# Kernel tuning notes

Measured on AMD Instinct MI355X. Metric: run time of the kernel, lower is better.

## Reference

```python
import jax, jax.numpy as jnp
import numpy as np

B, IMG, P, C, DEPTH, NCLS = 8, 224, 16, 96, 12, 43
H = W = IMG // P
L = H * W            # 196 tokens
D = 2 * C            # d_inner, ssm_ratio=2
N = 16               # d_state
R = (C + 15) // 16   # dt_rank = ceil(96/16) = 6
K = 4                # scan directions


def _ln(x, w, b, eps=1e-6):
    mu = x.mean(-1, keepdims=True)
    var = ((x - mu) ** 2).mean(-1, keepdims=True)
    return (x - mu) * jax.lax.rsqrt(var + eps) * w + b


def setup_inputs() -> dict:
    key = jax.random.key(0)
    ks = jax.random.split(key, 16)
    def nrm(k, shape, s=0.02):
        return jax.random.normal(k, shape, jnp.float32) * s
    return {
        "x": jax.random.normal(ks[0], (B, 3, IMG, IMG), jnp.float32),
        "patch_w": nrm(ks[1], (C, 3, P, P)),
        "patch_b": jnp.zeros((C,), jnp.float32),
        "pos_embed": nrm(ks[2], (1, L, C)),
        "ln1_w": jnp.ones((DEPTH, C), jnp.float32),
        "ln1_b": jnp.zeros((DEPTH, C), jnp.float32),
        "in_proj_w": nrm(ks[3], (DEPTH, C, 2 * D)),
        "conv_w": nrm(ks[4], (DEPTH, D, 1, 3, 3), 0.1),
        "conv_b": jnp.zeros((DEPTH, D), jnp.float32),
        "x_proj_w": nrm(ks[5], (DEPTH, K, R + 2 * N, D)),
        "dt_proj_w": nrm(ks[6], (DEPTH, K, D, R), R ** -0.5),
        "dt_proj_b": jnp.full((DEPTH, K, D), float(np.log(np.expm1(0.01))), jnp.float32),
        "A_logs": jnp.tile(jnp.log(jnp.arange(1, N + 1, dtype=jnp.float32)), (DEPTH, K, D, 1)),
        "Ds": jnp.ones((DEPTH, K, D), jnp.float32),
        "out_norm_w": jnp.ones((DEPTH, D), jnp.float32),
        "out_norm_b": jnp.zeros((DEPTH, D), jnp.float32),
        "out_proj_w": nrm(ks[7], (DEPTH, D, C)),
        "norm_w": jnp.ones((C,), jnp.float32),
        "norm_b": jnp.zeros((C,), jnp.float32),
        "head_w": nrm(ks[8], (C, NCLS)),
        "head_b": jnp.zeros((NCLS,), jnp.float32),
    }


def _ss2d(x, in_w, cw, cb, xpw, dtw, dtb, Alog, Dsk, onw, onb, ow):
    # x: (B,H,W,C)  -- SS2D 'v2' forward
    xz = x @ in_w                          # (B,H,W,2D)
    xa, z = jnp.split(xz, 2, axis=-1)
    xc = jnp.transpose(xa, (0, 3, 1, 2))   # (B,D,H,W)
    xc = jax.lax.conv_general_dilated(xc, cw, (1, 1), "SAME",
        dimension_numbers=("NCHW", "OIHW", "NCHW"), feature_group_count=D)
    xc = jax.nn.silu(xc + cb[None, :, None, None])
    # cross-scan: 4 traversal orders (row-major, col-major, and their reverses)
    x1 = xc.reshape(-1, D, L)
    x2 = jnp.transpose(xc, (0, 1, 3, 2)).reshape(-1, D, L)
    xs = jnp.stack([x1, x2, x1[..., ::-1], x2[..., ::-1]], 1)   # (B,K,D,L)
    dbl = jnp.einsum("bkdl,kcd->bkcl", xs, xpw)
    dts, Bs, Cs = jnp.split(dbl, [R, R + N], axis=2)            # (B,K,R,L),(B,K,N,L),(B,K,N,L)
    dts = jnp.einsum("bkrl,kdr->bkdl", dts, dtw)
    dts = jax.nn.softplus(dts + dtb[None, :, :, None])
    A = -jnp.exp(Alog)                                          # (K,D,N)
    # selective scan over token axis (sequential recurrence)
    seq = (jnp.moveaxis(xs, -1, 0), jnp.moveaxis(dts, -1, 0),
           jnp.moveaxis(Bs, -1, 0), jnp.moveaxis(Cs, -1, 0))
    h0 = jnp.zeros(xs.shape[:3] + (N,), xs.dtype)               # (B,K,D,N)
    def step(h, t):
        x_t, dt_t, B_t, C_t = t
        h = h * jnp.exp(dt_t[..., None] * A) + (dt_t * x_t)[..., None] * B_t[:, :, None, :]
        return h, jnp.einsum("bkdn,bkn->bkd", h, C_t)
    _, ys = jax.lax.scan(step, h0, seq)
    ys = jnp.moveaxis(ys, 0, -1)                                # (B,K,D,L)
    ys = ys + Dsk[None, :, :, None] * xs
    # cross-merge: undo reverses/transpose and sum the 4 directions
    y = ys[:, 0] + ys[:, 2, :, ::-1]
    yt = ys[:, 1] + ys[:, 3, :, ::-1]
    y = y + jnp.transpose(yt.reshape(-1, D, W, H), (0, 1, 3, 2)).reshape(-1, D, L)
    y = jnp.transpose(y.reshape(-1, D, H, W), (0, 2, 3, 1))     # (B,H,W,D)
    y = _ln(y, onw, onb)
    y = y * jax.nn.silu(z)
    return y @ ow


def reference(x, patch_w, patch_b, pos_embed, ln1_w, ln1_b, in_proj_w, conv_w, conv_b,
              x_proj_w, dt_proj_w, dt_proj_b, A_logs, Ds, out_norm_w, out_norm_b,
              out_proj_w, norm_w, norm_b, head_w, head_b):
    # patch embed: 16x16 stride-16 conv -> (B, L, C)
    t = jax.lax.conv_general_dilated(x, patch_w, (P, P), "VALID",
        dimension_numbers=("NCHW", "OIHW", "NCHW")) + patch_b[None, :, None, None]
    t = jnp.transpose(t.reshape(-1, C, L), (0, 2, 1)) + pos_embed
    t = t.reshape(-1, H, W, C)
    for i in range(DEPTH):
        t = t + _ss2d(_ln(t, ln1_w[i], ln1_b[i]), in_proj_w[i], conv_w[i], conv_b[i],
                      x_proj_w[i], dt_proj_w[i], dt_proj_b[i], A_logs[i], Ds[i],
                      out_norm_w[i], out_norm_b[i], out_proj_w[i])
    t = _ln(t.reshape(-1, L, C), norm_w, norm_b)
    return t.mean(1) @ head_w + head_b
```

## Files before the change

kernel.cpp:

```cpp
#include <hip/hip_runtime.h>
#include <math.h>

#define BB 8
#define IMGS 224
#define PSZ 16
#define CC 96
#define DEPTH 12
#define NCLS 43
#define HH 14
#define WW 14
#define LL 196
#define DD 192
#define NSTATE 16
#define RRANK 6
#define KDIR 4
#define DBLC 38
#define NSEG 16
#define PTOK 4
#define TSTR 200
#define OFF_B 1200
#define OFF_C 4336
#define DBKSZ 7552
#define XT 14
#define XPAD 196
#define GT 4
#define YSTRIDE (BB * DD * LL)

__device__ __forceinline__ float wave_sum(float v) {
#pragma unroll
  for (int m = 32; m; m >>= 1) v += __shfl_xor(v, m, 64);
  return v;
}

__device__ __forceinline__ float silu_f(float x) {
  return x / (1.f + __expf(-x));
}

__global__ void k_patch(const float* __restrict__ x, const float* __restrict__ pw,
                        const float* __restrict__ pb, const float* __restrict__ pos,
                        float* __restrict__ t) {
  __shared__ float s_x[PTOK][768];
  int tok0 = blockIdx.x * PTOK;
  for (int tk = 0; tk < PTOK; tk++) {
    int tok = tok0 + tk;
    int b = tok / LL, l = tok % LL;
    int ph = l / WW, pwc = l % WW;
    for (int e = threadIdx.x; e < 768; e += 128) {
      int ci = e >> 8, kh = (e >> 4) & 15, kw = e & 15;
      s_x[tk][e] = x[((size_t)(b * 3 + ci) * IMGS + ph * PSZ + kh) * IMGS + pwc * PSZ + kw];
    }
  }
  __syncthreads();
  if (threadIdx.x < CC) {
    int c = threadIdx.x;
    float a0 = pb[c], a1 = a0, a2 = a0, a3 = a0;
    const float* wr = pw + (size_t)c * 768;
    for (int e = 0; e < 768; e++) {
      float wv = wr[e];
      a0 += s_x[0][e] * wv;
      a1 += s_x[1][e] * wv;
      a2 += s_x[2][e] * wv;
      a3 += s_x[3][e] * wv;
    }
    float acc[4] = {a0, a1, a2, a3};
    for (int tk = 0; tk < PTOK; tk++) {
      int tok = tok0 + tk;
      t[(size_t)tok * CC + c] = acc[tk] + pos[(tok % LL) * CC + c];
    }
  }
}

__global__ void k_lnproj(const float* __restrict__ t, const float* __restrict__ w,
                         const float* __restrict__ bias, const float* __restrict__ ipw,
                         float* __restrict__ xa, float* __restrict__ z) {
  __shared__ float s_x[CC];
  int tok = blockIdx.x;
  int tid = threadIdx.x;
  if (tid < 64) {
    int lane = tid;
    const float* p = t + (size_t)tok * CC;
    float v0 = p[lane];
    float v1 = (lane < CC - 64) ? p[lane + 64] : 0.f;
    float mu = wave_sum(v0 + v1) * (1.f / CC);
    float d0 = v0 - mu;
    float d1 = (lane < CC - 64) ? (v1 - mu) : 0.f;
    float var = wave_sum(d0 * d0 + d1 * d1) * (1.f / CC);
    float rs = rsqrtf(var + 1e-6f);
    s_x[lane] = d0 * rs * w[lane] + bias[lane];
    if (lane < CC - 64) s_x[lane + 64] = d1 * rs * w[lane + 64] + bias[lane + 64];
  }
  __syncthreads();
  int j = tid;
  float acc = 0.f;
  for (int c = 0; c < CC; c++) acc += s_x[c] * ipw[(size_t)c * (2 * DD) + j];
  if (j < DD) xa[(size_t)tok * DD + j] = acc;
  else z[(size_t)tok * DD + (j - DD)] = acc;
}

__global__ __launch_bounds__(256, 4) void k_xproj(
    const float* __restrict__ xa, const float* __restrict__ cw,
    const float* __restrict__ cb, const float* __restrict__ xpw,
    float* __restrict__ xcT, float* __restrict__ dbl) {
  __shared__ float s_w[DBLC * DD];
  __shared__ float s_x[XT * XPAD];
  int lt = blockIdx.x;
  int k = blockIdx.y;
  int b = blockIdx.z;
  int tid = threadIdx.x;
  int l0 = lt * XT;

  const float4* wsrc = (const float4*)(xpw + (size_t)k * DBLC * DD);
  float4* wdst = (float4*)s_w;
  for (int idx = tid; idx < (DBLC * DD) / 4; idx += 256) wdst[idx] = wsrc[idx];

  for (int idx = tid; idx < XT * (DD / 4); idx += 256) {
    int i = idx / (DD / 4);
    int d = (idx % (DD / 4)) * 4;
    int l = l0 + i;
    int lr = (k >= 2) ? (LL - 1 - l) : l;
    int src = (k & 1) ? ((lr % HH) * WW + lr / HH) : lr;
    int h = src / WW, w = src % WW;
    const float4 bv = *(const float4*)(cb + d);
    float a0 = bv.x, a1 = bv.y, a2 = bv.z, a3 = bv.w;
    if (h >= 1 && h < HH - 1 && w >= 1 && w < WW - 1) {
#pragma unroll
      for (int kh = 0; kh < 3; kh++) {
#pragma unroll
        for (int kw = 0; kw < 3; kw++) {
          const float4 v = *(const float4*)(
              xa + ((size_t)(b * LL + (h + kh - 1) * WW + (w + kw - 1))) * DD + d);
          int wo = kh * 3 + kw;
          a0 += v.x * cw[(d + 0) * 9 + wo];
          a1 += v.y * cw[(d + 1) * 9 + wo];
          a2 += v.z * cw[(d + 2) * 9 + wo];
          a3 += v.w * cw[(d + 3) * 9 + wo];
        }
      }
    } else {
      for (int kh = 0; kh < 3; kh++) {
        int hh = h + kh - 1;
        if (hh < 0 || hh >= HH) continue;
        for (int kw = 0; kw < 3; kw++) {
          int ww = w + kw - 1;
          if (ww < 0 || ww >= WW) continue;
          const float4 v = *(const float4*)(xa + ((size_t)(b * LL + hh * WW + ww)) * DD + d);
          int wo = kh * 3 + kw;
          a0 += v.x * cw[(d + 0) * 9 + wo];
          a1 += v.y * cw[(d + 1) * 9 + wo];
          a2 += v.z * cw[(d + 2) * 9 + wo];
          a3 += v.w * cw[(d + 3) * 9 + wo];
        }
      }
    }
    float4 r = make_float4(silu_f(a0), silu_f(a1), silu_f(a2), silu_f(a3));
    *(float4*)(s_x + i * XPAD + d) = r;
    if (k == 0) *(float4*)(xcT + ((size_t)(b * LL) + src) * DD + d) = r;
  }
  __syncthreads();

  int li = tid & 15;
  int cbi = tid >> 4;
  if (li >= XT) return;
  int l = l0 + li;
  float* base = dbl + (size_t)(b * KDIR + k) * DBKSZ;
  const float4* xr = (const float4*)(s_x + li * XPAD);
  const float4* w0 = (const float4*)(s_w + cbi * DD);
  const float4* w1 = (const float4*)(s_w + (cbi + 16) * DD);
  bool has2 = (cbi < DBLC - 32);
  const float4* w2 = has2 ? (const float4*)(s_w + (cbi + 32) * DD) : w0;
  float a0 = 0.f, a1 = 0.f, a2 = 0.f;
#pragma unroll 8
  for (int q = 0; q < DD / 4; q++) {
    float4 a = xr[q];
    float4 v0 = w0[q], v1 = w1[q], v2 = w2[q];
    a0 += a.x * v0.x + a.y * v0.y + a.z * v0.z + a.w * v0.w;
    a1 += a.x * v1.x + a.y * v1.y + a.z * v1.z + a.w * v1.w;
    a2 += a.x * v2.x + a.y * v2.y + a.z * v2.z + a.w * v2.w;
  }
  {
    int c = cbi;
    if (c < RRANK) base[c * TSTR + l] = a0;
    else base[OFF_B + l * NSTATE + (c - RRANK)] = a0;
  }
  {
    int c = cbi + 16;
    if (c < RRANK + NSTATE) base[OFF_B + l * NSTATE + (c - RRANK)] = a1;
    else base[OFF_C + (c - RRANK - NSTATE) * TSTR + l] = a1;
  }
  if (has2) {
    int c = cbi + 32;
    base[OFF_C + (c - RRANK - NSTATE) * TSTR + l] = a2;
  }
}

__global__ __launch_bounds__(256, 4) void k_scan(
    const float* __restrict__ xcT, const float* __restrict__ dbl,
    const float* __restrict__ dtw, const float* __restrict__ dtb,
    const float* __restrict__ alog, const float* __restrict__ dsv,
    float* __restrict__ ysum) {
  __shared__ float s_h[2][NSTATE][LL + 1];
  __shared__ float s_dt[2][LL];
  __shared__ float s_u[2][LL];
  __shared__ float s_xv[2][LL];
  __shared__ float s_cumdt[2][LL];
  __shared__ unsigned short s_src[LL];
  __shared__ float s_hin[2][NSEG][NSTATE];
  __shared__ float s_hend[2][NSEG][NSTATE];
  __shared__ float s_cum[2][NSEG][NSTATE];
  __shared__ float s_segsum[2][NSEG];
  __shared__ float s_A[2][NSTATE];
  __shared__ float s_y[2][LL];
  int tid = threadIdx.x;
  int s = tid >> 4;
  int n = tid & 15;
  int bd = blockIdx.x;
  int dp = bd % (DD / 2);
  int d0 = dp * 2;
  int b = bd / (DD / 2);
  int k = blockIdx.y;

  int len = (s < 4) ? 13 : 12;
  int l0 = s * 12 + ((s < 4) ? s : 4);

  float A0 = -__expf(alog[((size_t)k * DD + d0) * NSTATE + n]);
  float A1 = -__expf(alog[((size_t)k * DD + d0 + 1) * NSTATE + n]);
  float Dsc0 = dsv[k * DD + d0];
  float Dsc1 = dsv[k * DD + d0 + 1];
  const float* blp = dbl + (size_t)(b * KDIR + k) * DBKSZ;
  if (tid < NSTATE) { s_A[0][tid] = A0; s_A[1][tid] = A1; }

  if (tid < LL) {
    int l = tid;
    float r[RRANK];
#pragma unroll
    for (int rr = 0; rr < RRANK; rr++) r[rr] = blp[rr * TSTR + l];
    const float* wp0 = dtw + ((size_t)k * DD + d0) * RRANK;
    const float* wp1 = wp0 + RRANK;
    float m0 = dtb[k * DD + d0], m1 = dtb[k * DD + d0 + 1];
#pragma unroll
    for (int rr = 0; rr < RRANK; rr++) { m0 += r[rr] * wp0[rr]; m1 += r[rr] * wp1[rr]; }
    float dt0 = (m0 > 20.f) ? m0 : __logf(1.f + __expf(m0));
    float dt1 = (m1 > 20.f) ? m1 : __logf(1.f + __expf(m1));
    int lr = (k >= 2) ? (LL - 1 - l) : l;
    int src = (k & 1) ? ((lr % HH) * WW + lr / HH) : lr;
    float2 xv = *(const float2*)(xcT + ((size_t)b * LL + src) * DD + d0);
    s_dt[0][l] = dt0; s_dt[1][l] = dt1;
    s_u[0][l] = dt0 * xv.x; s_u[1][l] = dt1 * xv.y;
    s_xv[0][l] = xv.x; s_xv[1][l] = xv.y;
    s_src[l] = (unsigned short)src;
  }
  __syncthreads();

  if (tid < LL) {
    int l = tid;
    int myseg = (l < 52) ? (l / 13) : (4 + (l - 52) / 12);
    int sl0 = myseg * 12 + ((myseg < 4) ? myseg : 4);
    float a0 = 0.f, a1 = 0.f;
    for (int j = sl0; j <= l; j++) { a0 += s_dt[0][j]; a1 += s_dt[1][j]; }
    s_cumdt[0][l] = a0; s_cumdt[1][l] = a1;
    int slen = (myseg < 4) ? 13 : 12;
    if (l == sl0 + slen - 1) { s_segsum[0][myseg] = a0; s_segsum[1][myseg] = a1; }
  }
  __syncthreads();

  float Breg[13];
#pragma unroll
  for (int i = 0; i < 13; i++) {
    int li = (i < len) ? (l0 + i) : l0;
    Breg[i] = blp[OFF_B + li * NSTATE + n];
  }
  float h0 = 0.f, h1 = 0.f;
#pragma unroll
  for (int i = 0; i < 13; i++) {
    if (i < len) {
      int l = l0 + i;
      float a0 = __expf(s_dt[0][l] * A0);
      float a1 = __expf(s_dt[1][l] * A1);
      h0 = h0 * a0 + s_u[0][l] * Breg[i];
      h1 = h1 * a1 + s_u[1][l] * Breg[i];
      s_h[0][n][l] = h0;
      s_h[1][n][l] = h1;
    }
  }
  s_hend[0][s][n] = h0; s_hend[1][s][n] = h1;
  s_cum[0][s][n] = __expf(A0 * s_segsum[0][s]);
  s_cum[1][s][n] = __expf(A1 * s_segsum[1][s]);
  __syncthreads();

  {
    float hh0 = 0.f, hh1 = 0.f;
    for (int ss = 0; ss < s; ss++) {
      hh0 = s_cum[0][ss][n] * hh0 + s_hend[0][ss][n];
      hh1 = s_cum[1][ss][n] * hh1 + s_hend[1][ss][n];
    }
    s_hin[0][s][n] = hh0; s_hin[1][s][n] = hh1;
  }
  __syncthreads();

  if (tid < LL) {
    int l = tid;
    int myseg = (l < 52) ? (l / 13) : (4 + (l - 52) / 12);
    float cd0 = s_cumdt[0][l], cd1 = s_cumdt[1][l];
    const float* q = blp + OFF_C + l;
    float y0 = 0.f, y1 = 0.f;
#pragma unroll
    for (int nn = 0; nn < NSTATE; nn++) {
      float Cv = q[nn * TSTR];
      float hf0 = s_h[0][nn][l] + __expf(s_A[0][nn] * cd0) * s_hin[0][myseg][nn];
      float hf1 = s_h[1][nn][l] + __expf(s_A[1][nn] * cd1) * s_hin[1][myseg][nn];
      y0 += hf0 * Cv;
      y1 += hf1 * Cv;
    }
    y0 += Dsc0 * s_xv[0][l];
    y1 += Dsc1 * s_xv[1][l];
    int src = s_src[l];
    s_y[0][src] = y0;
    s_y[1][src] = y1;
  }
  __syncthreads();
  if (tid < LL) {
    size_t base = (size_t)k * YSTRIDE + ((size_t)b * DD + d0) * LL;
    ysum[base + tid] = s_y[0][tid];
    ysum[base + LL + tid] = s_y[1][tid];
  }
}

__global__ void k_gateproj(const float* __restrict__ ys,
                           const float* __restrict__ onw, const float* __restrict__ onb,
                           const float* __restrict__ z, const float* __restrict__ opw,
                           float* __restrict__ t,
                           const float* __restrict__ nlw, const float* __restrict__ nlb,
                           const float* __restrict__ ipw,
                           float* __restrict__ xa, float* __restrict__ zout, int mode) {
  __shared__ float s_g[GT][DD];
  __shared__ float s_t[GT][CC];
  __shared__ float s_x[GT][CC];
  __shared__ float s_p[4][GT][CC];
  int tok0 = blockIdx.x * GT;
  int b = tok0 / LL;
  int l0 = tok0 % LL;
  int tid = threadIdx.x;

  if (tid < DD) {
    size_t base = ((size_t)b * DD + tid) * LL + l0;
    float4 v0 = *(const float4*)(ys + base);
    float4 v1 = *(const float4*)(ys + (size_t)YSTRIDE + base);
    float4 v2 = *(const float4*)(ys + 2 * (size_t)YSTRIDE + base);
    float4 v3 = *(const float4*)(ys + 3 * (size_t)YSTRIDE + base);
    s_g[0][tid] = v0.x + v1.x + v2.x + v3.x;
    s_g[1][tid] = v0.y + v1.y + v2.y + v3.y;
    s_g[2][tid] = v0.z + v1.z + v2.z + v3.z;
    s_g[3][tid] = v0.w + v1.w + v2.w + v3.w;
  }
  __syncthreads();

  {
    int w = tid >> 6;
    int lane = tid & 63;
    if (w < GT) {
      int tok = tok0 + w;
      float v0 = s_g[w][lane];
      float v1 = s_g[w][lane + 64];
      float v2 = s_g[w][lane + 128];
      float mu = wave_sum(v0 + v1 + v2) * (1.f / DD);
      float d0 = v0 - mu, d1 = v1 - mu, d2 = v2 - mu;
      float var = wave_sum(d0 * d0 + d1 * d1 + d2 * d2) * (1.f / DD);
      float rs = rsqrtf(var + 1e-6f);
      const float* zp = z + (size_t)tok * DD;
      s_g[w][lane]       = (d0 * rs * onw[lane] + onb[lane]) * silu_f(zp[lane]);
      s_g[w][lane + 64]  = (d1 * rs * onw[lane + 64] + onb[lane + 64]) * silu_f(zp[lane + 64]);
      s_g[w][lane + 128] = (d2 * rs * onw[lane + 128] + onb[lane + 128]) * silu_f(zp[lane + 128]);
    }
  }
  __syncthreads();

  {
    int c = tid % CC;
    int part = tid / CC;
    int dlo = part * 48;
    float a0 = 0.f, a1 = 0.f, a2 = 0.f, a3 = 0.f;
#pragma unroll 8
    for (int j = 0; j < 48; j++) {
      float wv = opw[(size_t)(dlo + j) * CC + c];
      a0 += s_g[0][dlo + j] * wv;
      a1 += s_g[1][dlo + j] * wv;
      a2 += s_g[2][dlo + j] * wv;
      a3 += s_g[3][dlo + j] * wv;
    }
    s_p[part][0][c] = a0;
    s_p[part][1][c] = a1;
    s_p[part][2][c] = a2;
    s_p[part][3][c] = a3;
  }
  __syncthreads();
  {
    int tk = tid / CC;
    int c = tid % CC;
    float tn = t[(size_t)(tok0 + tk) * CC + c] +
               s_p[0][tk][c] + s_p[1][tk][c] + s_p[2][tk][c] + s_p[3][tk][c];
    t[(size_t)(tok0 + tk) * CC + c] = tn;
    s_t[tk][c] = tn;
  }
  __syncthreads();

  {
    int w = tid >> 6;
    int lane = tid & 63;
    if (w < GT) {
      float v0 = s_t[w][lane];
      float v1 = (lane < CC - 64) ? s_t[w][lane + 64] : 0.f;
      float mu2 = wave_sum(v0 + v1) * (1.f / CC);
      float d0 = v0 - mu2;
      float d1 = (lane < CC - 64) ? (v1 - mu2) : 0.f;
      float var2 = wave_sum(d0 * d0 + d1 * d1) * (1.f / CC);
      float rs2 = rsqrtf(var2 + 1e-6f);
      s_x[w][lane] = d0 * rs2 * nlw[lane] + nlb[lane];
      if (lane < CC - 64) s_x[w][lane + 64] = d1 * rs2 * nlw[lane + 64] + nlb[lane + 64];
    }
  }
  __syncthreads();

  if (mode == 2) {
    int tk = tid / CC;
    int c = tid % CC;
    xa[(size_t)(tok0 + tk) * CC + c] = s_x[tk][c] * (1.f / LL);
    return;
  }

  {
    float b0 = 0.f, b1 = 0.f, b2 = 0.f, b3 = 0.f;
    for (int c = 0; c < CC; c++) {
      float wv = ipw[(size_t)c * (2 * DD) + tid];
      b0 += s_x[0][c] * wv;
      b1 += s_x[1][c] * wv;
      b2 += s_x[2][c] * wv;
      b3 += s_x[3][c] * wv;
    }
    float acc[GT] = {b0, b1, b2, b3};
#pragma unroll
    for (int tk = 0; tk < GT; tk++) {
      int tok = tok0 + tk;
      if (tid < DD) xa[(size_t)tok * DD + tid] = acc[tk];
      else zout[(size_t)tok * DD + (tid - DD)] = acc[tk];
    }
  }
}

__global__ void k_head(const float* __restrict__ t2, const float* __restrict__ hw,
                       const float* __restrict__ hb, float* __restrict__ out) {
  __shared__ float s_part[2][CC];
  __shared__ float s_pool[CC];
  int b = blockIdx.x;
  int tid = threadIdx.x;
  if (tid < 2 * CC) {
    int part = tid / CC;
    int c = tid % CC;
    int l0 = part * 98;
    float acc = 0.f;
    for (int i = 0; i < 98; i++) acc += t2[((size_t)b * LL + l0 + i) * CC + c];
    s_part[part][c] = acc;
  }
  __syncthreads();
  if (tid < CC) s_pool[tid] = s_part[0][tid] + s_part[1][tid];
  __syncthreads();
  if (tid < NCLS) {
    float acc = hb[tid];
    for (int c = 0; c < CC; c++) acc += s_pool[c] * hw[c * NCLS + tid];
    out[b * NCLS + tid] = acc;
  }
}

extern "C" void kernel_launch(void* const* d_in, const int* in_sizes, int n_in,
                              void* d_out, int out_size, void* d_ws, size_t ws_size,
                              hipStream_t stream) {
  const float* x       = (const float*)d_in[0];
  const float* patch_w = (const float*)d_in[1];
  const float* patch_b = (const float*)d_in[2];
  const float* pos     = (const float*)d_in[3];
  const float* ln1_w   = (const float*)d_in[4];
  const float* ln1_b   = (const float*)d_in[5];
  const float* ipw     = (const float*)d_in[6];
  const float* cw      = (const float*)d_in[7];
  const float* cb      = (const float*)d_in[8];
  const float* xpw     = (const float*)d_in[9];
  const float* dtw     = (const float*)d_in[10];
  const float* dtb     = (const float*)d_in[11];
  const float* alog    = (const float*)d_in[12];
  const float* dsp     = (const float*)d_in[13];
  const float* onw     = (const float*)d_in[14];
  const float* onb     = (const float*)d_in[15];
  const float* opw     = (const float*)d_in[16];
  const float* nw      = (const float*)d_in[17];
  const float* nb      = (const float*)d_in[18];
  const float* hw      = (const float*)d_in[19];
  const float* hb      = (const float*)d_in[20];
  float* out = (float*)d_out;

  float* wsf  = (float*)d_ws;
  float* t    = wsf;
  float* xa   = t    + BB * LL * CC;
  float* z    = xa   + BB * LL * DD;
  float* xcT  = z    + BB * LL * DD;
  float* dbl  = xcT  + BB * LL * DD;
  float* ysum = dbl  + BB * KDIR * DBKSZ;
  float* t2   = ysum + (size_t)KDIR * YSTRIDE;

  k_patch<<<BB * LL / PTOK, 128, 0, stream>>>(x, patch_w, patch_b, pos, t);
  k_lnproj<<<BB * LL, 384, 0, stream>>>(t, ln1_w, ln1_b, ipw, xa, z);

  for (int i = 0; i < DEPTH; i++) {
    k_xproj<<<dim3(LL / XT, KDIR, BB), 256, 0, stream>>>(
        xa, cw + i * DD * 9, cb + i * DD,
        xpw + (size_t)i * KDIR * DBLC * DD, xcT, dbl);
    k_scan<<<dim3(BB * DD / 2, KDIR), 256, 0, stream>>>(
        xcT, dbl, dtw + (size_t)i * KDIR * DD * RRANK, dtb + i * KDIR * DD,
        alog + (size_t)i * KDIR * DD * NSTATE, dsp + i * KDIR * DD, ysum);
    if (i < DEPTH - 1) {
      k_gateproj<<<BB * LL / GT, 384, 0, stream>>>(
          ysum, onw + i * DD, onb + i * DD, z, opw + (size_t)i * DD * CC, t,
          ln1_w + (i + 1) * CC, ln1_b + (i + 1) * CC, ipw + (size_t)(i + 1) * CC * 2 * DD,
          xa, z, 1);
    } else {
      k_gateproj<<<BB * LL / GT, 384, 0, stream>>>(
          ysum, onw + i * DD, onb + i * DD, z, opw + (size_t)i * DD * CC, t,
          nw, nb, ipw, t2, z, 2);
    }
  }

  k_head<<<BB, 256, 0, stream>>>(t2, hw, hb, out);
}
```

Baseline: 762.4 us.

## Fuse patch embed with first LN/in-proj and drop scan state buffer

Merges the patch-embedding kernel with the first layernorm and input projection into one kernel, processing four tokens per block with a split-K patch reduction. In the scan kernel, the per-timestep hidden-state shared buffer is removed. The C-weighted sum over states is now done with wave shuffles inside the sequential loop, and the segment-carry correction is added in a second shuffle pass. This cuts LDS usage and raises occupancy hints, at the cost of extra shuffle reductions on the serial path.

```diff
diff --git a/kernel.cpp b/kernel.cpp
--- a/kernel.cpp
+++ b/kernel.cpp
@@ -36,65 +36,99 @@
   return x / (1.f + __expf(-x));
 }
 
-__global__ void k_patch(const float* __restrict__ x, const float* __restrict__ pw,
-                        const float* __restrict__ pb, const float* __restrict__ pos,
-                        float* __restrict__ t) {
-  __shared__ float s_x[PTOK][768];
+__global__ void k_patchln(const float* __restrict__ x, const float* __restrict__ pw,
+                          const float* __restrict__ pb, const float* __restrict__ pos,
+                          const float* __restrict__ lw, const float* __restrict__ lb,
+                          const float* __restrict__ ipw,
+                          float* __restrict__ t, float* __restrict__ xa,
+                          float* __restrict__ z) {
+  __shared__ float s_px[PTOK][768];
+  __shared__ float s_part[2][PTOK][CC];
+  __shared__ float s_t[PTOK][CC];
+  __shared__ float s_xn[PTOK][CC];
   int tok0 = blockIdx.x * PTOK;
+  int tid = threadIdx.x;
+
   for (int tk = 0; tk < PTOK; tk++) {
     int tok = tok0 + tk;
     int b = tok / LL, l = tok % LL;
     int ph = l / WW, pwc = l % WW;
-    for (int e = threadIdx.x; e < 768; e += 128) {
+    for (int e = tid; e < 768; e += 256) {
       int ci = e >> 8, kh = (e >> 4) & 15, kw = e & 15;
-      s_x[tk][e] = x[((size_t)(b * 3 + ci) * IMGS + ph * PSZ + kh) * IMGS + pwc * PSZ + kw];
-    }
-  }
-  __syncthreads();
-  if (threadIdx.x < CC) {
-    int c = threadIdx.x;
-    float a0 = pb[c], a1 = a0, a2 = a0, a3 = a0;
-    const float* wr = pw + (size_t)c * 768;
-    for (int e = 0; e < 768; e++) {
+      s_px[tk][e] = x[((size_t)(b * 3 + ci) * IMGS + ph * PSZ + kh) * IMGS + pwc * PSZ + kw];
+    }
+  }
+  __syncthreads();
+
+  if (tid < 2 * CC) {
+    int c = tid % CC, eh = tid / CC;
+    const float* wr = pw + (size_t)c * 768 + eh * 384;
+    const float* p0 = &s_px[0][eh * 384];
+    const float* p1 = &s_px[1][eh * 384];
+    const float* p2 = &s_px[2][eh * 384];
+    const float* p3 = &s_px[3][eh * 384];
+    float a0 = 0.f, a1 = 0.f, a2 = 0.f, a3 = 0.f;
+    for (int e = 0; e < 384; e++) {
       float wv = wr[e];
-      a0 += s_x[0][e] * wv;
-      a1 += s_x[1][e] * wv;
-      a2 += s_x[2][e] * wv;
-      a3 += s_x[3][e] * wv;
-    }
-    float acc[4] = {a0, a1, a2, a3};
-    for (int tk = 0; tk < PTOK; tk++) {
-      int tok = tok0 + tk;
-      t[(size_t)tok * CC + c] = acc[tk] + pos[(tok % LL) * CC + c];
-    }
-  }
-}
-
-__global__ void k_lnproj(const float* __restrict__ t, const float* __restrict__ w,
-                         const float* __restrict__ bias, const float* __restrict__ ipw,
-                         float* __restrict__ xa, float* __restrict__ z) {
-  __shared__ float s_x[CC];
-  int tok = blockIdx.x;
-  int tid = threadIdx.x;
-  if (tid < 64) {
-    int lane = tid;
-    const float* p = t + (size_t)tok * CC;
-    float v0 = p[lane];
-    float v1 = (lane < CC - 64) ? p[lane + 64] : 0.f;
+      a0 += p0[e] * wv;
+      a1 += p1[e] * wv;
+      a2 += p2[e] * wv;
+      a3 += p3[e] * wv;
+    }
+    s_part[eh][0][c] = a0;
+    s_part[eh][1][c] = a1;
+    s_part[eh][2][c] = a2;
+    s_part[eh][3][c] = a3;
+  }
+  __syncthreads();
+
+  for (int idx = tid; idx < PTOK * CC; idx += 256) {
+    int tk = idx / CC, c = idx % CC;
+    int tok = tok0 + tk;
+    float v = s_part[0][tk][c] + s_part[1][tk][c] + pb[c] + pos[(tok % LL) * CC + c];
+    t[(size_t)tok * CC + c] = v;
+    s_t[tk][c] = v;
+  }
+  __syncthreads();
+
+  {
+    int w = tid >> 6;
+    int lane = tid & 63;
+    float v0 = s_t[w][lane];
+    float v1 = (lane < CC - 64) ? s_t[w][lane + 64] : 0.f;
     float mu = wave_sum(v0 + v1) * (1.f / CC);
     float d0 = v0 - mu;
     float d1 = (lane < CC - 64) ? (v1 - mu) : 0.f;
     float var = wave_sum(d0 * d0 + d1 * d1) * (1.f / CC);
     float rs = rsqrtf(var + 1e-6f);
-    s_x[lane] = d0 * rs * w[lane] + bias[lane];
-    if (lane < CC - 64) s_x[lane + 64] = d1 * rs * w[lane + 64] + bias[lane + 64];
-  }
-  __syncthreads();
-  int j = tid;
-  float acc = 0.f;
-  for (int c = 0; c < CC; c++) acc += s_x[c] * ipw[(size_t)c * (2 * DD) + j];
-  if (j < DD) xa[(size_t)tok * DD + j] = acc;
-  else z[(size_t)tok * DD + (j - DD)] = acc;
+    s_xn[w][lane] = d0 * rs * lw[lane] + lb[lane];
+    if (lane < CC - 64) s_xn[w][lane + 64] = d1 * rs * lw[lane + 64] + lb[lane + 64];
+  }
+  __syncthreads();
+
+  {
+    bool two = tid < (2 * DD - 256);
+    float b0 = 0.f, b1 = 0.f, b2 = 0.f, b3 = 0.f;
+    float c0 = 0.f, c1 = 0.f, c2 = 0.f, c3 = 0.f;
+    for (int c = 0; c < CC; c++) {
+      float x0 = s_xn[0][c], x1 = s_xn[1][c], x2 = s_xn[2][c], x3 = s_xn[3][c];
+      float wv = ipw[(size_t)c * (2 * DD) + tid];
+      b0 += x0 * wv; b1 += x1 * wv; b2 += x2 * wv; b3 += x3 * wv;
+      if (two) {
+        float wv2 = ipw[(size_t)c * (2 * DD) + tid + 256];
+        c0 += x0 * wv2; c1 += x1 * wv2; c2 += x2 * wv2; c3 += x3 * wv2;
+      }
+    }
+    float accb[PTOK] = {b0, b1, b2, b3};
+    float accc[PTOK] = {c0, c1, c2, c3};
+#pragma unroll
+    for (int tk = 0; tk < PTOK; tk++) {
+      int tok = tok0 + tk;
+      if (tid < DD) xa[(size_t)tok * DD + tid] = accb[tk];
+      else z[(size_t)tok * DD + (tid - DD)] = accb[tk];
+      if (two) z[(size_t)tok * DD + (tid + 256 - DD)] = accc[tk];
+    }
+  }
 }
 
 __global__ __launch_bounds__(256, 4) void k_xproj(
@@ -193,12 +227,11 @@
   }
 }
 
-__global__ __launch_bounds__(256, 4) void k_scan(
+__global__ __launch_bounds__(256, 6) void k_scan(
     const float* __restrict__ xcT, const float* __restrict__ dbl,
     const float* __restrict__ dtw, const float* __restrict__ dtb,
     const float* __restrict__ alog, const float* __restrict__ dsv,
     float* __restrict__ ysum) {
-  __shared__ float s_h[2][NSTATE][LL + 1];
   __shared__ float s_dt[2][LL];
   __shared__ float s_u[2][LL];
   __shared__ float s_xv[2][LL];
@@ -208,8 +241,8 @@
   __shared__ float s_hend[2][NSEG][NSTATE];
   __shared__ float s_cum[2][NSEG][NSTATE];
   __shared__ float s_segsum[2][NSEG];
-  __shared__ float s_A[2][NSTATE];
-  __shared__ float s_y[2][LL];
+  __shared__ float s_yl[2][LL];
+  __shared__ float s_yf[2][LL];
   int tid = threadIdx.x;
   int s = tid >> 4;
   int n = tid & 15;
@@ -227,7 +260,6 @@
   float Dsc0 = dsv[k * DD + d0];
   float Dsc1 = dsv[k * DD + d0 + 1];
   const float* blp = dbl + (size_t)(b * KDIR + k) * DBKSZ;
-  if (tid < NSTATE) { s_A[0][tid] = A0; s_A[1][tid] = A1; }
 
   if (tid < LL) {
     int l = tid;
@@ -263,6 +295,7 @@
   }
   __syncthreads();
 
+  const float* crow = blp + OFF_C + n * TSTR;
   float Breg[13];
 #pragma unroll
   for (int i = 0; i < 13; i++) {
@@ -278,8 +311,14 @@
       float a1 = __expf(s_dt[1][l] * A1);
       h0 = h0 * a0 + s_u[0][l] * Breg[i];
       h1 = h1 * a1 + s_u[1][l] * Breg[i];
-      s_h[0][n][l] = h0;
-      s_h[1][n][l] = h1;
+      float Cv = crow[l];
+      float t0 = h0 * Cv, t1 = h1 * Cv;
+#pragma unroll
+      for (int m = 1; m < 16; m <<= 1) {
+        t0 += __shfl_xor(t0, m, 64);
+        t1 += __shfl_xor(t1, m, 64);
+      }
+      if (n == 0) { s_yl[0][l] = t0; s_yl[1][l] = t1; }
     }
   }
   s_hend[0][s][n] = h0; s_hend[1][s][n] = h1;
@@ -297,31 +336,33 @@
   }
   __syncthreads();
 
-  if (tid < LL) {
-    int l = tid;
-    int myseg = (l < 52) ? (l / 13) : (4 + (l - 52) / 12);
-    float cd0 = s_cumdt[0][l], cd1 = s_cumdt[1][l];
-    const float* q = blp + OFF_C + l;
-    float y0 = 0.f, y1 = 0.f;
-#pragma unroll
-    for (int nn = 0; nn < NSTATE; nn++) {
-      float Cv = q[nn * TSTR];
-      float hf0 = s_h[0][nn][l] + __expf(s_A[0][nn] * cd0) * s_hin[0][myseg][nn];
-      float hf1 = s_h[1][nn][l] + __expf(s_A[1][nn] * cd1) * s_hin[1][myseg][nn];
-      y0 += hf0 * Cv;
-      y1 += hf1 * Cv;
-    }
-    y0 += Dsc0 * s_xv[0][l];
-    y1 += Dsc1 * s_xv[1][l];
-    int src = s_src[l];
-    s_y[0][src] = y0;
-    s_y[1][src] = y1;
+  {
+    float hin0 = s_hin[0][s][n], hin1 = s_hin[1][s][n];
+#pragma unroll
+    for (int i = 0; i < 13; i++) {
+      if (i < len) {
+        int l = l0 + i;
+        float Cv = crow[l];
+        float t0 = __expf(A0 * s_cumdt[0][l]) * hin0 * Cv;
+        float t1 = __expf(A1 * s_cumdt[1][l]) * hin1 * Cv;
+#pragma unroll
+        for (int m = 1; m < 16; m <<= 1) {
+          t0 += __shfl_xor(t0, m, 64);
+          t1 += __shfl_xor(t1, m, 64);
+        }
+        if (n == 0) {
+          int sr = s_src[l];
+          s_yf[0][sr] = s_yl[0][l] + t0 + Dsc0 * s_xv[0][l];
+          s_yf[1][sr] = s_yl[1][l] + t1 + Dsc1 * s_xv[1][l];
+        }
+      }
+    }
   }
   __syncthreads();
   if (tid < LL) {
     size_t base = (size_t)k * YSTRIDE + ((size_t)b * DD + d0) * LL;
-    ysum[base + tid] = s_y[0][tid];
-    ysum[base + LL + tid] = s_y[1][tid];
+    ysum[base + tid] = s_yf[0][tid];
+    ysum[base + LL + tid] = s_yf[1][tid];
   }
 }
 
@@ -505,8 +546,8 @@
   float* ysum = dbl  + BB * KDIR * DBKSZ;
   float* t2   = ysum + (size_t)KDIR * YSTRIDE;
 
-  k_patch<<<BB * LL / PTOK, 128, 0, stream>>>(x, patch_w, patch_b, pos, t);
-  k_lnproj<<<BB * LL, 384, 0, stream>>>(t, ln1_w, ln1_b, ipw, xa, z);
+  k_patchln<<<BB * LL / PTOK, 256, 0, stream>>>(x, patch_w, patch_b, pos,
+                                                ln1_w, ln1_b, ipw, t, xa, z);
 
   for (int i = 0; i < DEPTH; i++) {
     k_xproj<<<dim3(LL / XT, KDIR, BB), 256, 0, stream>>>(
```

New measurement: 1.068 ms. 1.4x slower.

## Cut LDS footprint in x-projection and scan kernels to raise occupancy

Applied to the files above, without the earlier changes.

The x-projection kernel no longer stages the 38x192 weight slice in shared memory. It reads the weights as float4 directly from global memory and relies on cache reuse, and its minimum-occupancy launch hint is dropped. The scan kernel keeps only one direction's hidden-state history in LDS and holds the other in registers. It computes the output for the two channels in two sequential passes, reuses the dt buffer for outputs, and raises its occupancy hint to 6. The intent is to lower per-block LDS so more blocks fit per CU, at the cost of extra barriers, a second C-load pass, more registers, and uncached-in-LDS weight reads.

```diff
diff --git a/kernel.cpp b/kernel.cpp
--- a/kernel.cpp
+++ b/kernel.cpp
@@ -97,21 +97,16 @@
   else z[(size_t)tok * DD + (j - DD)] = acc;
 }
 
-__global__ __launch_bounds__(256, 4) void k_xproj(
+__global__ __launch_bounds__(256) void k_xproj(
     const float* __restrict__ xa, const float* __restrict__ cw,
     const float* __restrict__ cb, const float* __restrict__ xpw,
     float* __restrict__ xcT, float* __restrict__ dbl) {
-  __shared__ float s_w[DBLC * DD];
   __shared__ float s_x[XT * XPAD];
   int lt = blockIdx.x;
   int k = blockIdx.y;
   int b = blockIdx.z;
   int tid = threadIdx.x;
   int l0 = lt * XT;
-
-  const float4* wsrc = (const float4*)(xpw + (size_t)k * DBLC * DD);
-  float4* wdst = (float4*)s_w;
-  for (int idx = tid; idx < (DBLC * DD) / 4; idx += 256) wdst[idx] = wsrc[idx];
 
   for (int idx = tid; idx < XT * (DD / 4); idx += 256) {
     int i = idx / (DD / 4);
@@ -163,11 +158,12 @@
   if (li >= XT) return;
   int l = l0 + li;
   float* base = dbl + (size_t)(b * KDIR + k) * DBKSZ;
+  const float* wk = xpw + (size_t)k * DBLC * DD;
   const float4* xr = (const float4*)(s_x + li * XPAD);
-  const float4* w0 = (const float4*)(s_w + cbi * DD);
-  const float4* w1 = (const float4*)(s_w + (cbi + 16) * DD);
+  const float4* w0 = (const float4*)(wk + cbi * DD);
+  const float4* w1 = (const float4*)(wk + (cbi + 16) * DD);
   bool has2 = (cbi < DBLC - 32);
-  const float4* w2 = has2 ? (const float4*)(s_w + (cbi + 32) * DD) : w0;
+  const float4* w2 = has2 ? (const float4*)(wk + (cbi + 32) * DD) : w0;
   float a0 = 0.f, a1 = 0.f, a2 = 0.f;
 #pragma unroll 8
   for (int q = 0; q < DD / 4; q++) {
@@ -193,14 +189,13 @@
   }
 }
 
-__global__ __launch_bounds__(256, 4) void k_scan(
+__global__ __launch_bounds__(256, 6) void k_scan(
     const float* __restrict__ xcT, const float* __restrict__ dbl,
     const float* __restrict__ dtw, const float* __restrict__ dtb,
     const float* __restrict__ alog, const float* __restrict__ dsv,
     float* __restrict__ ysum) {
-  __shared__ float s_h[2][NSTATE][LL + 1];
-  __shared__ float s_dt[2][LL];
-  __shared__ float s_u[2][LL];
+  __shared__ float s_h[NSTATE][LL + 1];
+  __shared__ float s_dty[2][LL];
   __shared__ float s_xv[2][LL];
   __shared__ float s_cumdt[2][LL];
   __shared__ unsigned short s_src[LL];
@@ -209,7 +204,6 @@
   __shared__ float s_cum[2][NSEG][NSTATE];
   __shared__ float s_segsum[2][NSEG];
   __shared__ float s_A[2][NSTATE];
-  __shared__ float s_y[2][LL];
   int tid = threadIdx.x;
   int s = tid >> 4;
   int n = tid & 15;
@@ -244,8 +238,7 @@
     int lr = (k >= 2) ? (LL - 1 - l) : l;
     int src = (k & 1) ? ((lr % HH) * WW + lr / HH) : lr;
     float2 xv = *(const float2*)(xcT + ((size_t)b * LL + src) * DD + d0);
-    s_dt[0][l] = dt0; s_dt[1][l] = dt1;
-    s_u[0][l] = dt0 * xv.x; s_u[1][l] = dt1 * xv.y;
+    s_dty[0][l] = dt0; s_dty[1][l] = dt1;
     s_xv[0][l] = xv.x; s_xv[1][l] = xv.y;
     s_src[l] = (unsigned short)src;
   }
@@ -256,7 +249,7 @@
     int myseg = (l < 52) ? (l / 13) : (4 + (l - 52) / 12);
     int sl0 = myseg * 12 + ((myseg < 4) ? myseg : 4);
     float a0 = 0.f, a1 = 0.f;
-    for (int j = sl0; j <= l; j++) { a0 += s_dt[0][j]; a1 += s_dt[1][j]; }
+    for (int j = sl0; j <= l; j++) { a0 += s_dty[0][j]; a1 += s_dty[1][j]; }
     s_cumdt[0][l] = a0; s_cumdt[1][l] = a1;
     int slen = (myseg < 4) ? 13 : 12;
     if (l == sl0 + slen - 1) { s_segsum[0][myseg] = a0; s_segsum[1][myseg] = a1; }
@@ -269,17 +262,21 @@
     int li = (i < len) ? (l0 + i) : l0;
     Breg[i] = blp[OFF_B + li * NSTATE + n];
   }
+  float Hreg[13];
   float h0 = 0.f, h1 = 0.f;
 #pragma unroll
   for (int i = 0; i < 13; i++) {
     if (i < len) {
       int l = l0 + i;
-      float a0 = __expf(s_dt[0][l] * A0);
-      float a1 = __expf(s_dt[1][l] * A1);
-      h0 = h0 * a0 + s_u[0][l] * Breg[i];
-      h1 = h1 * a1 + s_u[1][l] * Breg[i];
-      s_h[0][n][l] = h0;
-      s_h[1][n][l] = h1;
+      float dt0 = s_dty[0][l], dt1 = s_dty[1][l];
+      float u0 = dt0 * s_xv[0][l];
+      float u1 = dt1 * s_xv[1][l];
+      float a0 = __expf(dt0 * A0);
+      float a1 = __expf(dt1 * A1);
+      h0 = h0 * a0 + u0 * Breg[i];
+      h1 = h1 * a1 + u1 * Breg[i];
+      s_h[n][l] = h0;
+      Hreg[i] = h1;
     }
   }
   s_hend[0][s][n] = h0; s_hend[1][s][n] = h1;
@@ -300,28 +297,47 @@
   if (tid < LL) {
     int l = tid;
     int myseg = (l < 52) ? (l / 13) : (4 + (l - 52) / 12);
-    float cd0 = s_cumdt[0][l], cd1 = s_cumdt[1][l];
+    float cd0 = s_cumdt[0][l];
     const float* q = blp + OFF_C + l;
-    float y0 = 0.f, y1 = 0.f;
+    float y0 = 0.f;
 #pragma unroll
     for (int nn = 0; nn < NSTATE; nn++) {
       float Cv = q[nn * TSTR];
-      float hf0 = s_h[0][nn][l] + __expf(s_A[0][nn] * cd0) * s_hin[0][myseg][nn];
-      float hf1 = s_h[1][nn][l] + __expf(s_A[1][nn] * cd1) * s_hin[1][myseg][nn];
+      float hf0 = s_h[nn][l] + __expf(s_A[0][nn] * cd0) * s_hin[0][myseg][nn];
       y0 += hf0 * Cv;
+    }
+    y0 += Dsc0 * s_xv[0][l];
+    s_dty[0][s_src[l]] = y0;
+  }
+  __syncthreads();
+
+#pragma unroll
+  for (int i = 0; i < 13; i++) {
+    if (i < len) s_h[n][l0 + i] = Hreg[i];
+  }
+  __syncthreads();
+
+  if (tid < LL) {
+    int l = tid;
+    int myseg = (l < 52) ? (l / 13) : (4 + (l - 52) / 12);
+    float cd1 = s_cumdt[1][l];
+    const float* q = blp + OFF_C + l;
+    float y1 = 0.f;
+#pragma unroll
+    for (int nn = 0; nn < NSTATE; nn++) {
+      float Cv = q[nn * TSTR];
+      float hf1 = s_h[nn][l] + __expf(s_A[1][nn] * cd1) * s_hin[1][myseg][nn];
       y1 += hf1 * Cv;
     }
-    y0 += Dsc0 * s_xv[0][l];
     y1 += Dsc1 * s_xv[1][l];
-    int src = s_src[l];
-    s_y[0][src] = y0;
-    s_y[1][src] = y1;
-  }
-  __syncthreads();
+    s_dty[1][s_src[l]] = y1;
+  }
+  __syncthreads();
+
   if (tid < LL) {
     size_t base = (size_t)k * YSTRIDE + ((size_t)b * DD + d0) * LL;
-    ysum[base + tid] = s_y[0][tid];
-    ysum[base + LL + tid] = s_y[1][tid];
+    ysum[base + tid] = s_dty[0][tid];
+    ysum[base + LL + tid] = s_dty[1][tid];
   }
 }
 
```

After: 791.6 us. 3.8% more time.
